# Kernel tuning notes

Hardware: AMD Instinct MI355X
Metric: run time of the kernel (lower is better)

The kernel has to match this reference:

```python
import jax, jax.numpy as jnp
import numpy as np

EPS = 1e-5

def _bn(x, g, b):
    # BatchNorm1d in training mode: stats over (batch, length) dims, biased var
    mean = jnp.mean(x, axis=(0, 2), keepdims=True)
    var = jnp.var(x, axis=(0, 2), keepdims=True)
    return (x - mean) * jax.lax.rsqrt(var + EPS) * g[None, :, None] + b[None, :, None]

def _conv1x1(x, w, b):
    # pointwise Conv1d: [B,C,T] x [O,C] -> [B,O,T]
    return jnp.einsum('bct,oc->bot', x, w) + b[None, :, None]

def setup_inputs() -> dict:
    key = jax.random.key(0)
    ks = jax.random.split(key, 4)
    B, C, T = 32, 1024, 2048
    x = jax.random.normal(ks[0], (B, C, T), dtype=jnp.float32)
    w1 = jax.random.normal(ks[1], (256, 1024), dtype=jnp.float32) * (1.0 / np.sqrt(1024))
    w2 = jax.random.normal(ks[2], (64, 256), dtype=jnp.float32) * (1.0 / np.sqrt(256))
    return {
        'x': x,
        'bn1_g': jnp.ones((1024,), jnp.float32), 'bn1_b': jnp.zeros((1024,), jnp.float32),
        'w1': w1, 'b1': jnp.zeros((256,), jnp.float32),
        'bn2_g': jnp.ones((256,), jnp.float32), 'bn2_b': jnp.zeros((256,), jnp.float32),
        'w2': w2, 'b2': jnp.zeros((64,), jnp.float32),
    }

def reference(x, bn1_g, bn1_b, w1, b1, bn2_g, bn2_b, w2, b2):
    # reduction layer: BN -> 1x1 conv -> ReLU (1024 -> 256)
    h = jax.nn.relu(_conv1x1(_bn(x, bn1_g, bn1_b), w1, b1))
    # out layer: BN -> 1x1 conv, no activation (256 -> 64)
    out = _conv1x1(_bn(h, bn2_g, bn2_b), w2, b2)
    o = out.shape[1]
    mu = out[:, : o // 2, :]
    logvar = out[:, o // 2 :, :]
    return (mu, logvar)
```

## Files before the change

### kernel.cpp

```cpp
#include <hip/hip_runtime.h>

#define B_  32
#define C1  1024
#define C2  256
#define T_  2048
#define EPSF 1e-5f
#define BPITCH 40

typedef __attribute__((ext_vector_type(8))) short bf16x8;
typedef __attribute__((ext_vector_type(4))) float f32x4;

static __device__ __forceinline__ unsigned short f2bf(float f) {
    union { float f; unsigned u; } v; v.f = f;
    unsigned r = v.u + 0x7fffu + ((v.u >> 16) & 1u);
    return (unsigned short)(r >> 16);
}
static __device__ __forceinline__ void g2l16(const void* g, void* l) {
    __builtin_amdgcn_global_load_lds(
        (const __attribute__((address_space(1))) unsigned int*)g,
        (__attribute__((address_space(3))) unsigned int*)l, 16, 0, 0);
}

__global__ __launch_bounds__(256) void k_stats(const float* __restrict__ x,
        float* __restrict__ psum, float* __restrict__ psq) {
    int ct = blockIdx.x, b = blockIdx.y, tid = threadIdx.x;
    int c0 = ct * 64;
    int cl = tid >> 2, t4 = tid & 3;
    const float* xrow = x + (size_t)b * C1 * T_ + (size_t)(c0 + cl) * T_ + t4 * 4;
    float s = 0.f, sq = 0.f;
    #pragma unroll 4
    for (int t0 = 0; t0 < T_; t0 += 16) {
        float4 v = *(const float4*)(xrow + t0);
        s  += v.x + v.y + v.z + v.w;
        sq += v.x * v.x + v.y * v.y + v.z * v.z + v.w * v.w;
    }
    s  += __shfl_xor(s, 1);  s  += __shfl_xor(s, 2);
    sq += __shfl_xor(sq, 1); sq += __shfl_xor(sq, 2);
    if (t4 == 0) {
        psum[(size_t)b * C1 + c0 + cl] = s;
        psq [(size_t)b * C1 + c0 + cl] = sq;
    }
}

__global__ __launch_bounds__(256) void k_bnstat1(const float* __restrict__ psum,
        const float* __restrict__ psq, const float* __restrict__ g1,
        const float* __restrict__ bb1, float* __restrict__ sc1, float* __restrict__ sh1) {
    int c = blockIdx.x * 256 + threadIdx.x;
    float s = 0.f, q = 0.f;
    for (int b = 0; b < B_; ++b) {
        s += psum[(size_t)b * C1 + c];
        q += psq[(size_t)b * C1 + c];
    }
    const float n = (float)(B_ * T_);
    float m = s / n;
    float sc = g1[c] * rsqrtf(q / n - m * m + EPSF);
    sc1[c] = sc;
    sh1[c] = bb1[c] - m * sc;
}

__global__ __launch_bounds__(256) void k_fold1(const float* __restrict__ w1,
        const float* __restrict__ b1, const float* __restrict__ sc1,
        const float* __restrict__ sh1, unsigned short* __restrict__ w1e,
        float* __restrict__ b1e) {
    int o = blockIdx.x, tid = threadIdx.x;
    int c = tid * 4;
    float4 w  = ((const float4*)(w1 + (size_t)o * C1))[tid];
    float4 sc = *(const float4*)(sc1 + c);
    float4 sh = *(const float4*)(sh1 + c);
    float p = w.x * sh.x + w.y * sh.y + w.z * sh.z + w.w * sh.w;
    uint2 pk;
    pk.x = (unsigned)f2bf(w.x * sc.x) | ((unsigned)f2bf(w.y * sc.y) << 16);
    pk.y = (unsigned)f2bf(w.z * sc.z) | ((unsigned)f2bf(w.w * sc.w) << 16);
    *((uint2*)(w1e + (size_t)o * C1 + c)) = pk;
    int wave = tid >> 6, lane = tid & 63;
    for (int m = 1; m < 64; m <<= 1) p += __shfl_xor(p, m);
    __shared__ float rs[4];
    if (lane == 0) rs[wave] = p;
    __syncthreads();
    if (tid == 0) b1e[o] = b1[o] + rs[0] + rs[1] + rs[2] + rs[3];
}

__global__ __launch_bounds__(256, 2) void k_gemm1(const float* __restrict__ x,
        const unsigned short* __restrict__ w1e, const float* __restrict__ b1e,
        unsigned short* __restrict__ hT, float* __restrict__ p2s, float* __restrict__ p2q) {
    __shared__ alignas(16) unsigned short sA[2][256 * 32];
    __shared__ alignas(16) unsigned short sB[2][128 * BPITCH];
    int bn = blockIdx.x, b = blockIdx.y;
    int tid = threadIdx.x;
    int wave = tid >> 6, lane = tid & 63;
    int wm = wave >> 1, wn = wave & 1;
    int l15 = lane & 15, q = lane >> 4;
    f32x4 acc[8][4] = {};

    int kk = tid >> 3, tc = tid & 7;
    const float* xbase = x + (size_t)b * C1 * T_ + (size_t)kk * T_ + (size_t)bn * 128 + tc * 4;

    auto stageA = [&](int buf, int k0) {
        #pragma unroll
        for (int i = 0; i < 4; ++i) {
            int idx = (wave * 4 + i) * 64 + lane;
            int row = idx >> 2, cq = idx & 3;
            g2l16(w1e + (size_t)row * C1 + k0 + cq * 8, &sA[buf][(wave * 4 + i) * 512]);
        }
    };
    float4 rB[4];
    auto loadB = [&](int k0) {
        #pragma unroll
        for (int j = 0; j < 4; ++j)
            rB[j] = *(const float4*)(xbase + (size_t)k0 * T_ + j * 32);
    };
    auto writeB = [&](int buf) {
        #pragma unroll
        for (int j = 0; j < 4; ++j) {
            int t = tc * 4 + j * 32;
            unsigned short* p = &sB[buf][t * BPITCH + kk];
            p[0 * BPITCH] = f2bf(rB[j].x);
            p[1 * BPITCH] = f2bf(rB[j].y);
            p[2 * BPITCH] = f2bf(rB[j].z);
            p[3 * BPITCH] = f2bf(rB[j].w);
        }
    };

    loadB(0);
    stageA(0, 0);
    writeB(0);
    __syncthreads();
    int cur = 0;
    for (int kt = 0; kt < 32; ++kt) {
        int nxt = cur ^ 1;
        if (kt < 31) {
            loadB((kt + 1) * 32);
            stageA(nxt, (kt + 1) * 32);
        }
        bf16x8 bfr[4];
        #pragma unroll
        for (int ni = 0; ni < 4; ++ni)
            bfr[ni] = *((const bf16x8*)&sB[cur][(wn * 64 + ni * 16 + l15) * BPITCH + q * 8]);
        #pragma unroll
        for (int mi = 0; mi < 8; ++mi) {
            bf16x8 af = *((const bf16x8*)&sA[cur][(wm * 128 + mi * 16 + l15) * 32 + q * 8]);
            #pragma unroll
            for (int ni = 0; ni < 4; ++ni)
                acc[mi][ni] = __builtin_amdgcn_mfma_f32_16x16x32_bf16(af, bfr[ni], acc[mi][ni], 0, 0, 0);
        }
        if (kt < 31) writeB(nxt);
        __syncthreads();
        cur = nxt;
    }
    int obase = wm * 128;
    int tbase = bn * 128 + wn * 64;
    int prow = (b * 16 + bn) * 2 + wn;
    #pragma unroll
    for (int mi = 0; mi < 8; ++mi) {
        int og = obase + mi * 16 + q * 4;
        float4 bias = *(const float4*)&b1e[og];
        float s0 = 0, s1 = 0, s2 = 0, s3 = 0, q0 = 0, q1 = 0, q2 = 0, q3 = 0;
        #pragma unroll
        for (int ni = 0; ni < 4; ++ni) {
            int t = tbase + ni * 16 + l15;
            float v0 = fmaxf(acc[mi][ni][0] + bias.x, 0.f);
            float v1 = fmaxf(acc[mi][ni][1] + bias.y, 0.f);
            float v2 = fmaxf(acc[mi][ni][2] + bias.z, 0.f);
            float v3 = fmaxf(acc[mi][ni][3] + bias.w, 0.f);
            s0 += v0; q0 += v0 * v0;  s1 += v1; q1 += v1 * v1;
            s2 += v2; q2 += v2 * v2;  s3 += v3; q3 += v3 * v3;
            uint2 pk;
            pk.x = (unsigned)f2bf(v0) | ((unsigned)f2bf(v1) << 16);
            pk.y = (unsigned)f2bf(v2) | ((unsigned)f2bf(v3) << 16);
            *(uint2*)&hT[((size_t)b * T_ + t) * C2 + og] = pk;
        }
        #pragma unroll
        for (int m = 1; m <= 8; m <<= 1) {
            s0 += __shfl_xor(s0, m); s1 += __shfl_xor(s1, m);
            s2 += __shfl_xor(s2, m); s3 += __shfl_xor(s3, m);
            q0 += __shfl_xor(q0, m); q1 += __shfl_xor(q1, m);
            q2 += __shfl_xor(q2, m); q3 += __shfl_xor(q3, m);
        }
        if (l15 == 0) {
            p2s[(size_t)(og + 0) * 1024 + prow] = s0;
            p2s[(size_t)(og + 1) * 1024 + prow] = s1;
            p2s[(size_t)(og + 2) * 1024 + prow] = s2;
            p2s[(size_t)(og + 3) * 1024 + prow] = s3;
            p2q[(size_t)(og + 0) * 1024 + prow] = q0;
            p2q[(size_t)(og + 1) * 1024 + prow] = q1;
            p2q[(size_t)(og + 2) * 1024 + prow] = q2;
            p2q[(size_t)(og + 3) * 1024 + prow] = q3;
        }
    }
}

__global__ __launch_bounds__(256) void k_bnstat2(const float* __restrict__ p2s,
        const float* __restrict__ p2q, const float* __restrict__ g2,
        const float* __restrict__ bb2, float* __restrict__ sc2, float* __restrict__ sh2) {
    int c = blockIdx.x, tid = threadIdx.x;
    float4 a  = *(const float4*)(p2s + (size_t)c * 1024 + tid * 4);
    float4 qv = *(const float4*)(p2q + (size_t)c * 1024 + tid * 4);
    float s = a.x + a.y + a.z + a.w;
    float q = qv.x + qv.y + qv.z + qv.w;
    for (int m = 1; m < 64; m <<= 1) { s += __shfl_xor(s, m); q += __shfl_xor(q, m); }
    __shared__ float rs[4], rq[4];
    int wave = tid >> 6, lane = tid & 63;
    if (lane == 0) { rs[wave] = s; rq[wave] = q; }
    __syncthreads();
    if (tid == 0) {
        s = rs[0] + rs[1] + rs[2] + rs[3];
        q = rq[0] + rq[1] + rq[2] + rq[3];
        const float n = (float)(B_ * T_);
        float m0 = s / n;
        float sc = g2[c] * rsqrtf(q / n - m0 * m0 + EPSF);
        sc2[c] = sc;
        sh2[c] = bb2[c] - m0 * sc;
    }
}

__global__ __launch_bounds__(256) void k_fold2(const float* __restrict__ w2,
        const float* __restrict__ b2, const float* __restrict__ sc2,
        const float* __restrict__ sh2, unsigned short* __restrict__ w2e,
        float* __restrict__ b2e) {
    int o = blockIdx.x, tid = threadIdx.x;
    float w = w2[(size_t)o * C2 + tid];
    w2e[(size_t)o * C2 + tid] = f2bf(w * sc2[tid]);
    float p = w * sh2[tid];
    int wave = tid >> 6, lane = tid & 63;
    for (int m = 1; m < 64; m <<= 1) p += __shfl_xor(p, m);
    __shared__ float rs[4];
    if (lane == 0) rs[wave] = p;
    __syncthreads();
    if (tid == 0) b2e[o] = b2[o] + rs[0] + rs[1] + rs[2] + rs[3];
}

__global__ __launch_bounds__(256) void k_gemm2(const unsigned short* __restrict__ hT,
        const unsigned short* __restrict__ w2e, const float* __restrict__ b2e,
        float* __restrict__ out) {
    __shared__ alignas(16) unsigned short sA[64 * 32];
    __shared__ alignas(16) unsigned short sB[128 * 32];
    int bn = blockIdx.x, b = blockIdx.y;
    int tid = threadIdx.x;
    int wave = tid >> 6, lane = tid & 63;
    int l15 = lane & 15, q = lane >> 4;
    f32x4 acc[4][2] = {};
    const unsigned short* hblk = hT + ((size_t)b * T_ + (size_t)bn * 128) * C2;

    for (int k0 = 0; k0 < C2; k0 += 32) {
        {
            int idx = wave * 64 + lane;
            int row = idx >> 2, cq = idx & 3;
            g2l16(w2e + (size_t)row * C2 + k0 + cq * 8, &sA[wave * 512]);
        }
        #pragma unroll
        for (int i = 0; i < 2; ++i) {
            int idx = (wave * 2 + i) * 64 + lane;
            int row = idx >> 2, cq = idx & 3;
            g2l16(hblk + (size_t)row * C2 + k0 + cq * 8, &sB[(wave * 2 + i) * 512]);
        }
        __syncthreads();
        bf16x8 af[4], bfr[2];
        #pragma unroll
        for (int mi = 0; mi < 4; ++mi)
            af[mi] = *((const bf16x8*)&sA[(mi * 16 + l15) * 32 + q * 8]);
        #pragma unroll
        for (int ni = 0; ni < 2; ++ni)
            bfr[ni] = *((const bf16x8*)&sB[(wave * 32 + ni * 16 + l15) * 32 + q * 8]);
        #pragma unroll
        for (int mi = 0; mi < 4; ++mi)
            #pragma unroll
            for (int ni = 0; ni < 2; ++ni)
                acc[mi][ni] = __builtin_amdgcn_mfma_f32_16x16x32_bf16(af[mi], bfr[ni], acc[mi][ni], 0, 0, 0);
        __syncthreads();
    }
    int tbase = bn * 128 + wave * 32;
    #pragma unroll
    for (int mi = 0; mi < 4; ++mi) {
        #pragma unroll
        for (int reg = 0; reg < 4; ++reg) {
            int o = mi * 16 + q * 4 + reg;
            float bias = b2e[o];
            size_t base = (o < 32)
                ? ((size_t)b * 32 * T_ + (size_t)o * T_)
                : (2097152u + (size_t)b * 32 * T_ + (size_t)(o - 32) * T_);
            #pragma unroll
            for (int ni = 0; ni < 2; ++ni) {
                int t = tbase + ni * 16 + l15;
                out[base + t] = acc[mi][ni][reg] + bias;
            }
        }
    }
}

extern "C" void kernel_launch(void* const* d_in, const int* in_sizes, int n_in,
                              void* d_out, int out_size, void* d_ws, size_t ws_size,
                              hipStream_t stream) {
    const float* x   = (const float*)d_in[0];
    const float* g1  = (const float*)d_in[1];
    const float* bb1 = (const float*)d_in[2];
    const float* w1  = (const float*)d_in[3];
    const float* b1  = (const float*)d_in[4];
    const float* g2  = (const float*)d_in[5];
    const float* bb2 = (const float*)d_in[6];
    const float* w2  = (const float*)d_in[7];
    const float* b2  = (const float*)d_in[8];
    float* out = (float*)d_out;

    char* ws = (char*)d_ws;
    float* b1e  = (float*)(ws + 0);
    float* b2e  = (float*)(ws + 4096);
    float* psum = (float*)(ws + 8192);
    float* psq  = (float*)(ws + 139264);
    float* p2s  = (float*)(ws + 270336);
    float* p2q  = (float*)(ws + 1318912);
    unsigned short* w1e = (unsigned short*)(ws + 2367488);
    unsigned short* w2e = (unsigned short*)(ws + 2891776);
    float* sc1 = (float*)(ws + 2924544);
    float* sh1 = (float*)(ws + 2928640);
    float* sc2 = (float*)(ws + 2932736);
    float* sh2 = (float*)(ws + 2933760);
    unsigned short* hT  = (unsigned short*)(ws + 2934784);

    k_stats  <<<dim3(16, 32), dim3(256), 0, stream>>>(x, psum, psq);
    k_bnstat1<<<dim3(4),      dim3(256), 0, stream>>>(psum, psq, g1, bb1, sc1, sh1);
    k_fold1  <<<dim3(256),    dim3(256), 0, stream>>>(w1, b1, sc1, sh1, w1e, b1e);
    k_gemm1  <<<dim3(16, 32), dim3(256), 0, stream>>>(x, w1e, b1e, hT, p2s, p2q);
    k_bnstat2<<<dim3(256),    dim3(256), 0, stream>>>(p2s, p2q, g2, bb2, sc2, sh2);
    k_fold2  <<<dim3(64),     dim3(256), 0, stream>>>(w2, b2, sc2, sh2, w2e, b2e);
    k_gemm2  <<<dim3(16, 32), dim3(256), 0, stream>>>(hT, w2e, b2e, out);
}
```

Before: 485.1 us.

## Merge all seven stages into one cooperative persistent kernel with grid syncs

Fuses the stats, BN-fold, GEMM1, stats2, fold2 and GEMM2 kernels into a single cooperative launch of 512 blocks. Stages are separated by grid-wide syncs, and shared memory is reused across phases. The aim is to remove the per-launch overhead and gaps of seven launches, since several of those kernels are tiny. It needs 2 blocks per CU to be co-resident, otherwise it falls back to the old path. Grid syncs can be costly, and idle blocks in the small phases waste time.

```diff
diff --git a/kernel.cpp b/kernel.cpp
--- a/kernel.cpp
+++ b/kernel.cpp
@@ -1,4 +1,7 @@
 #include <hip/hip_runtime.h>
+#include <hip/hip_cooperative_groups.h>
+
+namespace cg = cooperative_groups;
 
 #define B_  32
 #define C1  1024
@@ -20,6 +23,283 @@
         (const __attribute__((address_space(1))) unsigned int*)g,
         (__attribute__((address_space(3))) unsigned int*)l, 16, 0, 0);
 }
+
+__global__ __launch_bounds__(256, 2) void k_mega(
+        const float* __restrict__ x,
+        const float* __restrict__ g1, const float* __restrict__ bb1,
+        const float* __restrict__ w1, const float* __restrict__ b1,
+        const float* __restrict__ g2, const float* __restrict__ bb2,
+        const float* __restrict__ w2, const float* __restrict__ b2,
+        float* __restrict__ out,
+        float* __restrict__ psum, float* __restrict__ psq,
+        float* __restrict__ p2s, float* __restrict__ p2q,
+        unsigned short* __restrict__ w1e, unsigned short* __restrict__ w2e,
+        float* __restrict__ b1e, float* __restrict__ b2e,
+        float* __restrict__ sc1v, float* __restrict__ sh1v,
+        float* __restrict__ sc2v, float* __restrict__ sh2v,
+        unsigned short* __restrict__ hT) {
+    __shared__ alignas(16) unsigned char smem[53248];
+    cg::grid_group grid = cg::this_grid();
+    int bid = blockIdx.x, tid = threadIdx.x;
+    int wave = tid >> 6, lane = tid & 63;
+    const float n = (float)(B_ * T_);
+
+    {
+        int ct = bid & 15, b = bid >> 4;
+        int c0 = ct * 64;
+        int cl = tid >> 2, t4 = tid & 3;
+        const float* xrow = x + (size_t)b * C1 * T_ + (size_t)(c0 + cl) * T_ + t4 * 4;
+        float s = 0.f, sq = 0.f;
+        #pragma unroll 4
+        for (int t0 = 0; t0 < T_; t0 += 16) {
+            float4 v = *(const float4*)(xrow + t0);
+            s  += v.x + v.y + v.z + v.w;
+            sq += v.x * v.x + v.y * v.y + v.z * v.z + v.w * v.w;
+        }
+        s  += __shfl_xor(s, 1);  s  += __shfl_xor(s, 2);
+        sq += __shfl_xor(sq, 1); sq += __shfl_xor(sq, 2);
+        if (t4 == 0) {
+            psum[(size_t)b * C1 + c0 + cl] = s;
+            psq [(size_t)b * C1 + c0 + cl] = sq;
+        }
+    }
+    __threadfence();
+    grid.sync();
+
+    if (bid < 4) {
+        int c = bid * 256 + tid;
+        float s = 0.f, q = 0.f;
+        for (int b = 0; b < B_; ++b) {
+            s += psum[(size_t)b * C1 + c];
+            q += psq[(size_t)b * C1 + c];
+        }
+        float m = s / n;
+        float sc = g1[c] * rsqrtf(q / n - m * m + EPSF);
+        sc1v[c] = sc;
+        sh1v[c] = bb1[c] - m * sc;
+    }
+    __threadfence();
+    grid.sync();
+
+    if (bid < 256) {
+        float* rs = (float*)smem;
+        int o = bid;
+        int c = tid * 4;
+        float4 w  = ((const float4*)(w1 + (size_t)o * C1))[tid];
+        float4 sc = *(const float4*)(sc1v + c);
+        float4 sh = *(const float4*)(sh1v + c);
+        float p = w.x * sh.x + w.y * sh.y + w.z * sh.z + w.w * sh.w;
+        uint2 pk;
+        pk.x = (unsigned)f2bf(w.x * sc.x) | ((unsigned)f2bf(w.y * sc.y) << 16);
+        pk.y = (unsigned)f2bf(w.z * sc.z) | ((unsigned)f2bf(w.w * sc.w) << 16);
+        *((uint2*)(w1e + (size_t)o * C1 + c)) = pk;
+        float pr = p;
+        for (int m = 1; m < 64; m <<= 1) pr += __shfl_xor(pr, m);
+        if (lane == 0) rs[wave] = pr;
+        __syncthreads();
+        if (tid == 0) b1e[o] = b1[o] + rs[0] + rs[1] + rs[2] + rs[3];
+    }
+    __threadfence();
+    grid.sync();
+
+    {
+        unsigned short* sA = (unsigned short*)smem;
+        unsigned short* sB = (unsigned short*)(smem + 32768);
+        int bn = bid & 15, b = bid >> 4;
+        int wm = wave >> 1, wn = wave & 1;
+        int l15 = lane & 15, q = lane >> 4;
+        f32x4 acc[8][4] = {};
+        int kk = tid >> 3, tc = tid & 7;
+        const float* xbase = x + (size_t)b * C1 * T_ + (size_t)kk * T_ + (size_t)bn * 128 + tc * 4;
+
+        auto stageA = [&](int buf, int k0) {
+            #pragma unroll
+            for (int i = 0; i < 4; ++i) {
+                int idx = (wave * 4 + i) * 64 + lane;
+                int row = idx >> 2, cq = idx & 3;
+                g2l16(w1e + (size_t)row * C1 + k0 + cq * 8, sA + buf * 8192 + (wave * 4 + i) * 512);
+            }
+        };
+        float4 rB[4];
+        auto loadB = [&](int k0) {
+            #pragma unroll
+            for (int j = 0; j < 4; ++j)
+                rB[j] = *(const float4*)(xbase + (size_t)k0 * T_ + j * 32);
+        };
+        auto writeB = [&](int buf) {
+            #pragma unroll
+            for (int j = 0; j < 4; ++j) {
+                int t = tc * 4 + j * 32;
+                unsigned short* p = sB + buf * 5120 + t * BPITCH + kk;
+                p[0 * BPITCH] = f2bf(rB[j].x);
+                p[1 * BPITCH] = f2bf(rB[j].y);
+                p[2 * BPITCH] = f2bf(rB[j].z);
+                p[3 * BPITCH] = f2bf(rB[j].w);
+            }
+        };
+
+        loadB(0);
+        stageA(0, 0);
+        writeB(0);
+        __syncthreads();
+        int cur = 0;
+        for (int kt = 0; kt < 32; ++kt) {
+            int nxt = cur ^ 1;
+            if (kt < 31) {
+                loadB((kt + 1) * 32);
+                stageA(nxt, (kt + 1) * 32);
+            }
+            bf16x8 bfr[4];
+            #pragma unroll
+            for (int ni = 0; ni < 4; ++ni)
+                bfr[ni] = *((const bf16x8*)(sB + cur * 5120 + (wn * 64 + ni * 16 + l15) * BPITCH + q * 8));
+            #pragma unroll
+            for (int mi = 0; mi < 8; ++mi) {
+                bf16x8 af = *((const bf16x8*)(sA + cur * 8192 + (wm * 128 + mi * 16 + l15) * 32 + q * 8));
+                #pragma unroll
+                for (int ni = 0; ni < 4; ++ni)
+                    acc[mi][ni] = __builtin_amdgcn_mfma_f32_16x16x32_bf16(af, bfr[ni], acc[mi][ni], 0, 0, 0);
+            }
+            if (kt < 31) writeB(nxt);
+            __syncthreads();
+            cur = nxt;
+        }
+        int obase = wm * 128;
+        int tbase = bn * 128 + wn * 64;
+        int prow = (b * 16 + bn) * 2 + wn;
+        #pragma unroll
+        for (int mi = 0; mi < 8; ++mi) {
+            int og = obase + mi * 16 + q * 4;
+            float4 bias = *(const float4*)&b1e[og];
+            float s0 = 0, s1 = 0, s2 = 0, s3 = 0, q0 = 0, q1 = 0, q2 = 0, q3 = 0;
+            #pragma unroll
+            for (int ni = 0; ni < 4; ++ni) {
+                int t = tbase + ni * 16 + l15;
+                float v0 = fmaxf(acc[mi][ni][0] + bias.x, 0.f);
+                float v1 = fmaxf(acc[mi][ni][1] + bias.y, 0.f);
+                float v2 = fmaxf(acc[mi][ni][2] + bias.z, 0.f);
+                float v3 = fmaxf(acc[mi][ni][3] + bias.w, 0.f);
+                s0 += v0; q0 += v0 * v0;  s1 += v1; q1 += v1 * v1;
+                s2 += v2; q2 += v2 * v2;  s3 += v3; q3 += v3 * v3;
+                uint2 pk;
+                pk.x = (unsigned)f2bf(v0) | ((unsigned)f2bf(v1) << 16);
+                pk.y = (unsigned)f2bf(v2) | ((unsigned)f2bf(v3) << 16);
+                *(uint2*)&hT[((size_t)b * T_ + t) * C2 + og] = pk;
+            }
+            #pragma unroll
+            for (int m = 1; m <= 8; m <<= 1) {
+                s0 += __shfl_xor(s0, m); s1 += __shfl_xor(s1, m);
+                s2 += __shfl_xor(s2, m); s3 += __shfl_xor(s3, m);
+                q0 += __shfl_xor(q0, m); q1 += __shfl_xor(q1, m);
+                q2 += __shfl_xor(q2, m); q3 += __shfl_xor(q3, m);
+            }
+            if (l15 == 0) {
+                p2s[(size_t)(og + 0) * 1024 + prow] = s0;
+                p2s[(size_t)(og + 1) * 1024 + prow] = s1;
+                p2s[(size_t)(og + 2) * 1024 + prow] = s2;
+                p2s[(size_t)(og + 3) * 1024 + prow] = s3;
+                p2q[(size_t)(og + 0) * 1024 + prow] = q0;
+                p2q[(size_t)(og + 1) * 1024 + prow] = q1;
+                p2q[(size_t)(og + 2) * 1024 + prow] = q2;
+                p2q[(size_t)(og + 3) * 1024 + prow] = q3;
+            }
+        }
+    }
+    __threadfence();
+    grid.sync();
+
+    if (bid < 256) {
+        float* rs = (float*)smem;
+        float* rq = (float*)(smem + 16);
+        int c = bid;
+        float4 a  = *(const float4*)(p2s + (size_t)c * 1024 + tid * 4);
+        float4 qv = *(const float4*)(p2q + (size_t)c * 1024 + tid * 4);
+        float s = a.x + a.y + a.z + a.w;
+        float q = qv.x + qv.y + qv.z + qv.w;
+        for (int m = 1; m < 64; m <<= 1) { s += __shfl_xor(s, m); q += __shfl_xor(q, m); }
+        if (lane == 0) { rs[wave] = s; rq[wave] = q; }
+        __syncthreads();
+        if (tid == 0) {
+            s = rs[0] + rs[1] + rs[2] + rs[3];
+            q = rq[0] + rq[1] + rq[2] + rq[3];
+            float m0 = s / n;
+            float sc = g2[c] * rsqrtf(q / n - m0 * m0 + EPSF);
+            sc2v[c] = sc;
+            sh2v[c] = bb2[c] - m0 * sc;
+        }
+    }
+    __threadfence();
+    grid.sync();
+
+    if (bid < 64) {
+        float* rs = (float*)smem;
+        int o = bid;
+        float w = w2[(size_t)o * C2 + tid];
+        w2e[(size_t)o * C2 + tid] = f2bf(w * sc2v[tid]);
+        float p = w * sh2v[tid];
+        for (int m = 1; m < 64; m <<= 1) p += __shfl_xor(p, m);
+        if (lane == 0) rs[wave] = p;
+        __syncthreads();
+        if (tid == 0) b2e[o] = b2[o] + rs[0] + rs[1] + rs[2] + rs[3];
+    }
+    __threadfence();
+    grid.sync();
+
+    {
+        unsigned short* sA = (unsigned short*)smem;
+        unsigned short* sB = (unsigned short*)(smem + 4096);
+        int bn = bid & 15, b = bid >> 4;
+        int l15 = lane & 15, q = lane >> 4;
+        f32x4 acc[4][2] = {};
+        const unsigned short* hblk = hT + ((size_t)b * T_ + (size_t)bn * 128) * C2;
+
+        for (int k0 = 0; k0 < C2; k0 += 32) {
+            {
+                int idx = wave * 64 + lane;
+                int row = idx >> 2, cq = idx & 3;
+                g2l16(w2e + (size_t)row * C2 + k0 + cq * 8, sA + wave * 512);
+            }
+            #pragma unroll
+            for (int i = 0; i < 2; ++i) {
+                int idx = (wave * 2 + i) * 64 + lane;
+                int row = idx >> 2, cq = idx & 3;
+                g2l16(hblk + (size_t)row * C2 + k0 + cq * 8, sB + (wave * 2 + i) * 512);
+            }
+            __syncthreads();
+            bf16x8 af[4], bfr[2];
+            #pragma unroll
+            for (int mi = 0; mi < 4; ++mi)
+                af[mi] = *((const bf16x8*)(sA + (mi * 16 + l15) * 32 + q * 8));
+            #pragma unroll
+            for (int ni = 0; ni < 2; ++ni)
+                bfr[ni] = *((const bf16x8*)(sB + (wave * 32 + ni * 16 + l15) * 32 + q * 8));
+            #pragma unroll
+            for (int mi = 0; mi < 4; ++mi)
+                #pragma unroll
+                for (int ni = 0; ni < 2; ++ni)
+                    acc[mi][ni] = __builtin_amdgcn_mfma_f32_16x16x32_bf16(af[mi], bfr[ni], acc[mi][ni], 0, 0, 0);
+            __syncthreads();
+        }
+        int tbase = bn * 128 + wave * 32;
+        #pragma unroll
+        for (int mi = 0; mi < 4; ++mi) {
+            #pragma unroll
+            for (int reg = 0; reg < 4; ++reg) {
+                int o = mi * 16 + q * 4 + reg;
+                float bias = b2e[o];
+                size_t base = (o < 32)
+                    ? ((size_t)b * 32 * T_ + (size_t)o * T_)
+                    : (2097152u + (size_t)b * 32 * T_ + (size_t)(o - 32) * T_);
+                #pragma unroll
+                for (int ni = 0; ni < 2; ++ni) {
+                    int t = tbase + ni * 16 + l15;
+                    out[base + t] = acc[mi][ni][reg] + bias;
+                }
+            }
+        }
+    }
+}
+
 
 __global__ __launch_bounds__(256) void k_stats(const float* __restrict__ x,
         float* __restrict__ psum, float* __restrict__ psq) {
@@ -91,7 +371,6 @@
     int wm = wave >> 1, wn = wave & 1;
     int l15 = lane & 15, q = lane >> 4;
     f32x4 acc[8][4] = {};
-
     int kk = tid >> 3, tc = tid & 7;
     const float* xbase = x + (size_t)b * C1 * T_ + (size_t)kk * T_ + (size_t)bn * 128 + tc * 4;
 
@@ -245,22 +524,22 @@
         {
             int idx = wave * 64 + lane;
             int row = idx >> 2, cq = idx & 3;
-            g2l16(w2e + (size_t)row * C2 + k0 + cq * 8, &sA[wave * 512]);
+            g2l16(w2e + (size_t)row * C2 + k0 + cq * 8, sA + wave * 512);
         }
         #pragma unroll
         for (int i = 0; i < 2; ++i) {
             int idx = (wave * 2 + i) * 64 + lane;
             int row = idx >> 2, cq = idx & 3;
-            g2l16(hblk + (size_t)row * C2 + k0 + cq * 8, &sB[(wave * 2 + i) * 512]);
+            g2l16(hblk + (size_t)row * C2 + k0 + cq * 8, sB + (wave * 2 + i) * 512);
         }
         __syncthreads();
         bf16x8 af[4], bfr[2];
         #pragma unroll
         for (int mi = 0; mi < 4; ++mi)
-            af[mi] = *((const bf16x8*)&sA[(mi * 16 + l15) * 32 + q * 8]);
+            af[mi] = *((const bf16x8*)(sA + (mi * 16 + l15) * 32 + q * 8));
         #pragma unroll
         for (int ni = 0; ni < 2; ++ni)
-            bfr[ni] = *((const bf16x8*)&sB[(wave * 32 + ni * 16 + l15) * 32 + q * 8]);
+            bfr[ni] = *((const bf16x8*)(sB + (wave * 32 + ni * 16 + l15) * 32 + q * 8));
         #pragma unroll
         for (int mi = 0; mi < 4; ++mi)
             #pragma unroll
@@ -316,6 +595,20 @@
     float* sh2 = (float*)(ws + 2933760);
     unsigned short* hT  = (unsigned short*)(ws + 2934784);
 
+    int maxBlk = 0;
+    hipError_t qe = hipOccupancyMaxActiveBlocksPerMultiprocessor(
+        &maxBlk, (const void*)k_mega, 256, 0);
+    if (qe == hipSuccess && maxBlk >= 2) {
+        void* args[] = { (void*)&x, (void*)&g1, (void*)&bb1, (void*)&w1, (void*)&b1,
+                         (void*)&g2, (void*)&bb2, (void*)&w2, (void*)&b2, (void*)&out,
+                         (void*)&psum, (void*)&psq, (void*)&p2s, (void*)&p2q,
+                         (void*)&w1e, (void*)&w2e, (void*)&b1e, (void*)&b2e,
+                         (void*)&sc1, (void*)&sh1, (void*)&sc2, (void*)&sh2, (void*)&hT };
+        hipError_t le = hipLaunchCooperativeKernel((void*)k_mega, dim3(512), dim3(256),
+                                                   args, 0, stream);
+        if (le == hipSuccess) return;
+    }
+
     k_stats  <<<dim3(16, 32), dim3(256), 0, stream>>>(x, psum, psq);
     k_bnstat1<<<dim3(4),      dim3(256), 0, stream>>>(psum, psq, g1, bb1, sc1, sh1);
     k_fold1  <<<dim3(256),    dim3(256), 0, stream>>>(w1, b1, sc1, sh1, w1e, b1e);
```

Measured after the change: 483.2 us. No clear change (-0.4%).
